# Performance work log

Hardware: AMD Instinct MI355X
Metric: run time of the kernel (lower is better)

The kernel has to match this reference:

```python
import jax, jax.numpy as jnp
import numpy as np

WIN = 7
DIM = 384
HEADS = 12
HEAD_DIM = DIM // HEADS


def relative_position_index(win):
    ch = np.arange(win)
    cw = np.arange(win)
    coords = np.stack(np.meshgrid(ch, cw, indexing='ij'))  # [2,w,w]
    cf = coords.reshape(2, -1)
    rel = cf[:, :, None] - cf[:, None, :]  # [2,ww,ww]
    rel = rel.transpose(1, 2, 0)
    rel[:, :, 0] += win - 1
    rel[:, :, 1] += win - 1
    rel[:, :, 0] *= 2 * win - 1
    return jnp.array(rel.sum(-1), dtype=jnp.int32)  # [ww,ww]


def setup_inputs() -> dict:
    key = jax.random.key(0)
    ks = jax.random.split(key, 9)
    B, S = 1024, WIN * WIN
    M = 16  # windows per image
    s = 1.0 / np.sqrt(DIM)
    return {
        'hidden_states': jax.random.normal(ks[0], (B, S, DIM), jnp.float32),
        'attention_mask': jax.random.normal(ks[1], (M, S, S), jnp.float32),
        'Wq': jax.random.normal(ks[2], (DIM, DIM), jnp.float32) * s,
        'bq': jnp.zeros((DIM,), jnp.float32),
        'Wk': jax.random.normal(ks[3], (DIM, DIM), jnp.float32) * s,
        'bk': jnp.zeros((DIM,), jnp.float32),
        'Wv': jax.random.normal(ks[4], (DIM, DIM), jnp.float32) * s,
        'bv': jnp.zeros((DIM,), jnp.float32),
        'rel_bias_table': jax.random.normal(ks[5], ((2 * WIN - 1) ** 2, HEADS), jnp.float32) * 0.02,
        'rel_index': relative_position_index(WIN),
    }


def reference(hidden_states, attention_mask, Wq, bq, Wk, bk, Wv, bv, rel_bias_table, rel_index):
    B, S, _ = hidden_states.shape
    q = (hidden_states @ Wq + bq).reshape(B, S, HEADS, HEAD_DIM)
    k = (hidden_states @ Wk + bk).reshape(B, S, HEADS, HEAD_DIM)
    v = (hidden_states @ Wv + bv).reshape(B, S, HEADS, HEAD_DIM)
    q = q / jnp.sqrt(jnp.float32(HEAD_DIM)).astype(q.dtype)
    attn = jnp.einsum('bqhd,bkhd->bhqk', q, k)  # [B,H,S,S]
    # relative position bias: gather + reshape + transpose -> [1,H,S,S]
    bias = rel_bias_table[rel_index.reshape(-1)].reshape(S, S, HEADS)
    attn = attn + jnp.transpose(bias, (2, 0, 1))[None]
    # shifted-window mask add: [B//M, M, H, S, S]
    Mw = attention_mask.shape[0]
    attn = attn.reshape(B // Mw, Mw, HEADS, S, S) + attention_mask[None, :, None, :, :]
    attn = attn.reshape(B, HEADS, S, S)
    attn = jax.nn.softmax(attn, axis=-1)
    out = jnp.einsum('bhqk,bkhd->bqhd', attn, v).reshape(B, S, DIM)
    return out
```

## Files before the change

kernel.cpp:

```cpp
#include <hip/hip_runtime.h>

typedef __attribute__((ext_vector_type(8))) short short8;
typedef __attribute__((ext_vector_type(4))) float f32x4;
typedef __attribute__((ext_vector_type(4))) int i32x4;

__device__ __forceinline__ unsigned short f2bf(float f) {
  unsigned u = __builtin_bit_cast(unsigned, f);
  u += 0x7fffu + ((u >> 16) & 1u);
  return (unsigned short)(u >> 16);
}

__global__ __launch_bounds__(256) void k_prepw(const float* __restrict__ Wq, const float* __restrict__ Wk,
                                               const float* __restrict__ Wv, const float* __restrict__ bq,
                                               const float* __restrict__ bk, const float* __restrict__ bv,
                                               unsigned short* __restrict__ Wt, float* __restrict__ bvec) {
  int i = blockIdx.x * 256 + threadIdx.x;
  int n = i / 384, k = i - n * 384;
  int which = n / 384;
  int c = n - which * 384;
  const float* W = (which == 0) ? Wq : (which == 1) ? Wk : Wv;
  Wt[i] = f2bf(W[k * 384 + c]);
  if (k == 0) {
    const float* bb = (which == 0) ? bq : (which == 1) ? bk : bv;
    bvec[n] = bb[c];
  }
}

__global__ __launch_bounds__(256) void k_prept(const float* __restrict__ tab, const int* __restrict__ ridx,
                                               const float* __restrict__ am, float* __restrict__ T) {
  int i = blockIdx.x * 256 + threadIdx.x;
  int lane = i & 63;
  int rest = i >> 6;
  int ik = rest & 3, jq = (rest >> 2) & 3, wh = rest >> 4;
  int h = wh % 12, w = wh / 12;
  int lr = lane & 15, lg = lane >> 4;
  int q = jq * 16 + lr;
  f32x4 v;
  #pragma unroll
  for (int r = 0; r < 4; ++r) {
    int k = ik * 16 + lg * 4 + r;
    v[r] = (q < 49 && k < 49) ? tab[ridx[q * 49 + k] * 12 + h] + am[w * 2401 + q * 49 + k] : 0.f;
  }
  *(f32x4*)(T + (size_t)i * 4) = v;
}

__global__ __launch_bounds__(768, 3) void k_mega(const float* __restrict__ X,
                                                 const unsigned short* __restrict__ Wt,
                                                 const float* __restrict__ bvec,
                                                 const float* __restrict__ T,
                                                 float* __restrict__ out) {
  extern __shared__ unsigned short pool[];
  const int w = blockIdx.x;
  const int tid = threadIdx.x;
  const int lane = tid & 63, wid = tid >> 6;
  const int lr = lane & 15, lg = lane >> 4;
  char* poolB = (char*)pool;

  #pragma unroll
  for (int it = 0; it < 4; ++it) {
    int c = tid + 768 * it;
    int row = c / 48, c8 = c - row * 48;
    short8 v = {0, 0, 0, 0, 0, 0, 0, 0};
    if (row < 49) {
      const float* p = X + ((size_t)(w * 49 + row)) * 384 + c8 * 8;
      f32x4 f0 = *(const f32x4*)p;
      f32x4 f1 = *(const f32x4*)(p + 4);
      v[0] = (short)f2bf(f0[0]); v[1] = (short)f2bf(f0[1]); v[2] = (short)f2bf(f0[2]); v[3] = (short)f2bf(f0[3]);
      v[4] = (short)f2bf(f1[0]); v[5] = (short)f2bf(f1[1]); v[6] = (short)f2bf(f1[2]); v[7] = (short)f2bf(f1[3]);
    }
    *(short8*)(poolB + row * 768 + ((c8 * 16) ^ ((row & 7) << 4))) = v;
  }
  __syncthreads();

  const unsigned swz = (unsigned)((lr & 7) << 4);
  unsigned hq[16], hk[16], hv[16];
  {
    f32x4 acc[3][4][2] = {};
    const unsigned short* Bg0 = Wt + ((size_t)(0 * 384 + wid * 32 + lr)) * 384;
    const unsigned short* Bg1 = Wt + ((size_t)(1 * 384 + wid * 32 + lr)) * 384;
    const unsigned short* Bg2 = Wt + ((size_t)(2 * 384 + wid * 32 + lr)) * 384;
    short8 aC[4], bC[3][2], bN[3][2];
    bC[0][0] = *(const short8*)(Bg0 + lg * 8);
    bC[0][1] = *(const short8*)(Bg0 + 16 * 384 + lg * 8);
    bC[1][0] = *(const short8*)(Bg1 + lg * 8);
    bC[1][1] = *(const short8*)(Bg1 + 16 * 384 + lg * 8);
    bC[2][0] = *(const short8*)(Bg2 + lg * 8);
    bC[2][1] = *(const short8*)(Bg2 + 16 * 384 + lg * 8);
    #pragma unroll 2
    for (int k = 0; k < 12; ++k) {
      if (k < 11) {
        int ko = (k + 1) * 32 + lg * 8;
        bN[0][0] = *(const short8*)(Bg0 + ko);
        bN[0][1] = *(const short8*)(Bg0 + 16 * 384 + ko);
        bN[1][0] = *(const short8*)(Bg1 + ko);
        bN[1][1] = *(const short8*)(Bg1 + 16 * 384 + ko);
        bN[2][0] = *(const short8*)(Bg2 + ko);
        bN[2][1] = *(const short8*)(Bg2 + 16 * 384 + ko);
      }
      #pragma unroll
      for (int mi = 0; mi < 4; ++mi)
        aC[mi] = *(const short8*)(poolB + (16 * mi + lr) * 768 + (unsigned)((k * 64 + lg * 16) ^ swz));
      #pragma unroll
      for (int p = 0; p < 3; ++p)
        #pragma unroll
        for (int mi = 0; mi < 4; ++mi)
          #pragma unroll
          for (int ni = 0; ni < 2; ++ni)
            acc[p][mi][ni] = __builtin_amdgcn_mfma_f32_16x16x32_bf16(aC[mi], bC[p][ni], acc[p][mi][ni], 0, 0, 0);
      #pragma unroll
      for (int p = 0; p < 3; ++p) { bC[p][0] = bN[p][0]; bC[p][1] = bN[p][1]; }
    }
    #pragma unroll
    for (int p = 0; p < 3; ++p) {
      float scl = (p == 0) ? 0.17677669529663687f : 1.0f;
      unsigned* hd = (p == 0) ? hq : (p == 1) ? hk : hv;
      float b0 = bvec[p * 384 + wid * 32 + lr];
      float b1 = bvec[p * 384 + wid * 32 + 16 + lr];
      #pragma unroll
      for (int mi = 0; mi < 4; ++mi)
        #pragma unroll
        for (int ni = 0; ni < 2; ++ni) {
          float bb = ni ? b1 : b0;
          float v0 = (acc[p][mi][ni][0] + bb) * scl;
          float v1 = (acc[p][mi][ni][1] + bb) * scl;
          float v2 = (acc[p][mi][ni][2] + bb) * scl;
          float v3 = (acc[p][mi][ni][3] + bb) * scl;
          hd[(mi * 2 + ni) * 2 + 0] = (unsigned)f2bf(v0) | ((unsigned)f2bf(v1) << 16);
          hd[(mi * 2 + ni) * 2 + 1] = (unsigned)f2bf(v2) | ((unsigned)f2bf(v3) << 16);
        }
    }
  }
  __syncthreads();

  unsigned short* reg = pool + wid * 6400;
  unsigned short* Qs = reg;
  unsigned short* Ks = reg + 1984;
  unsigned short* Vt = reg + 4096;
  char* Pb = (char*)reg;
  #pragma unroll
  for (int mi = 0; mi < 4; ++mi)
    #pragma unroll
    for (int ni = 0; ni < 2; ++ni) {
      int d = ni * 16 + lr;
      #pragma unroll
      for (int e = 0; e < 2; ++e) {
        int s0 = 16 * mi + 4 * lg + 2 * e;
        *(unsigned*)&Vt[d * 72 + s0] = hv[(mi * 2 + ni) * 2 + e];
      }
      #pragma unroll
      for (int r = 0; r < 4; ++r) {
        int s = 16 * mi + 4 * lg + r;
        if (s < 49) {
          unsigned short qv = (unsigned short)(hq[(mi * 2 + ni) * 2 + (r >> 1)] >> ((r & 1) * 16));
          unsigned short kv = (unsigned short)(hk[(mi * 2 + ni) * 2 + (r >> 1)] >> ((r & 1) * 16));
          Qs[s * 40 + d] = qv;
          Ks[s * 40 + d] = kv;
        }
      }
    }

  short8 qf[4], kf[4];
  #pragma unroll
  for (int t = 0; t < 4; ++t) {
    int rq = t * 16 + lr; if (rq > 48) rq = 48;
    qf[t] = *(const short8*)&Qs[rq * 40 + lg * 8];
    kf[t] = *(const short8*)&Ks[rq * 40 + lg * 8];
  }
  f32x4 sc[4][4] = {};
  #pragma unroll
  for (int ik = 0; ik < 4; ++ik)
    #pragma unroll
    for (int jq = 0; jq < 4; ++jq)
      sc[ik][jq] = __builtin_amdgcn_mfma_f32_16x16x32_bf16(kf[ik], qf[jq], sc[ik][jq], 0, 0, 0);

  const float* Tb = T + ((size_t)((w & 15) * 12 + wid)) * 4096;
  #pragma unroll
  for (int jq = 0; jq < 4; ++jq) {
    #pragma unroll
    for (int ik = 0; ik < 4; ++ik) {
      f32x4 tv = *(const f32x4*)(Tb + ((jq * 4 + ik) * 64 + lane) * 4);
      #pragma unroll
      for (int r = 0; r < 4; ++r) {
        float v = sc[ik][jq][r] + tv[r];
        if (ik == 3) {
          if (r == 0) v = (lg == 0) ? v : -1e30f;
          else v = -1e30f;
        }
        sc[ik][jq][r] = v;
      }
    }
    float m = -1e30f;
    #pragma unroll
    for (int ik = 0; ik < 4; ++ik)
      #pragma unroll
      for (int r = 0; r < 4; ++r) m = fmaxf(m, sc[ik][jq][r]);
    m = fmaxf(m, __shfl_xor(m, 16));
    m = fmaxf(m, __shfl_xor(m, 32));
    float s = 0.f;
    #pragma unroll
    for (int ik = 0; ik < 4; ++ik)
      #pragma unroll
      for (int r = 0; r < 4; ++r) {
        float e = __expf(sc[ik][jq][r] - m);
        sc[ik][jq][r] = e;
        s += e;
      }
    s += __shfl_xor(s, 16);
    s += __shfl_xor(s, 32);
    float iv = 1.0f / s;
    int q = jq * 16 + lr;
    #pragma unroll
    for (int ik = 0; ik < 4; ++ik) {
      unsigned d0 = (unsigned)f2bf(sc[ik][jq][0] * iv) | ((unsigned)f2bf(sc[ik][jq][1] * iv) << 16);
      unsigned d1 = (unsigned)f2bf(sc[ik][jq][2] * iv) | ((unsigned)f2bf(sc[ik][jq][3] * iv) << 16);
      unsigned off = (unsigned)(q * 128 + ik * 32 + lg * 8) ^ ((unsigned)(lr & 7) << 4);
      *(uint2*)(Pb + off) = make_uint2(d0, d1);
    }
  }

  short8 vf[2][2];
  #pragma unroll
  for (int kk = 0; kk < 2; ++kk)
    #pragma unroll
    for (int nl = 0; nl < 2; ++nl)
      vf[kk][nl] = *(const short8*)&Vt[(nl * 16 + lr) * 72 + kk * 32 + lg * 8];
  f32x4 ao[4][2] = {};
  #pragma unroll
  for (int i = 0; i < 4; ++i) {
    short8 pf[2];
    #pragma unroll
    for (int kk = 0; kk < 2; ++kk) {
      unsigned off = (unsigned)((i * 16 + lr) * 128 + (kk * 4 + lg) * 16) ^ ((unsigned)(lr & 7) << 4);
      pf[kk] = *(const short8*)(Pb + off);
    }
    #pragma unroll
    for (int nl = 0; nl < 2; ++nl)
      #pragma unroll
      for (int kk = 0; kk < 2; ++kk)
        ao[i][nl] = __builtin_amdgcn_mfma_f32_16x16x32_bf16(pf[kk], vf[kk][nl], ao[i][nl], 0, 0, 0);
  }

  #pragma unroll
  for (int i = 0; i < 4; ++i) {
    #pragma unroll
    for (int j2 = 0; j2 < 4; ++j2) {
      int q = i * 16 + lg * 4 + j2;
      if (q < 49) {
        #pragma unroll
        for (int nl = 0; nl < 2; ++nl) {
          int d = nl * 16 + lr;
          out[((size_t)(w * 49 + q)) * 384 + wid * 32 + d] = ao[i][nl][j2];
        }
      }
    }
  }
}

extern "C" void kernel_launch(void* const* d_in, const int* in_sizes, int n_in,
                              void* d_out, int out_size, void* d_ws, size_t ws_size,
                              hipStream_t stream) {
  const float* hs  = (const float*)d_in[0];
  const float* am  = (const float*)d_in[1];
  const float* Wq  = (const float*)d_in[2];
  const float* bq  = (const float*)d_in[3];
  const float* Wk  = (const float*)d_in[4];
  const float* bk  = (const float*)d_in[5];
  const float* Wv  = (const float*)d_in[6];
  const float* bv  = (const float*)d_in[7];
  const float* tab = (const float*)d_in[8];
  const int*   rix = (const int*)d_in[9];
  float* out = (float*)d_out;
  char* ws = (char*)d_ws;

  size_t o = 0;
  auto alloc = [&](size_t bytes) { size_t r = o; o = (o + bytes + 255) & ~(size_t)255; return r; };
  unsigned short* Wt   = (unsigned short*)(ws + alloc(1152ull * 384 * 2));
  float*          bvec = (float*)(ws + alloc(1152ull * 4));
  float*          Tt   = (float*)(ws + alloc(192ull * 4096 * 4));
  (void)ws_size; (void)in_sizes; (void)n_in; (void)out_size;

  hipFuncSetAttribute((const void*)k_mega, hipFuncAttributeMaxDynamicSharedMemorySize, 153600);

  k_prepw<<<1728, 256, 0, stream>>>(Wq, Wk, Wv, bq, bk, bv, Wt, bvec);
  k_prept<<<768, 256, 0, stream>>>(tab, rix, am, Tt);
  k_mega<<<1024, 768, 153600, stream>>>(hs, Wt, bvec, Tt, out);
}
```

Baseline: 296.4 us.

## Split each window across two blocks of six heads and restructure QKV GEMM loop

Each 12-head window is now handled by two 384-thread blocks, each owning 6 heads, so shared memory per block halves and two blocks can be resident per CU. The QKV projection loop now processes one projection at a time with a 4-deep rotating prefetch buffer for weight fragments, and wraps the MFMA bursts in s_setprio. The intent is to let the staging, GEMM and attention phases of different blocks overlap, and to ease register pressure. In exchange, each window's input rows are loaded from global memory and converted to bf16 twice, once per block.

```diff
diff --git a/kernel.cpp b/kernel.cpp
--- a/kernel.cpp
+++ b/kernel.cpp
@@ -2,7 +2,6 @@
 
 typedef __attribute__((ext_vector_type(8))) short short8;
 typedef __attribute__((ext_vector_type(4))) float f32x4;
-typedef __attribute__((ext_vector_type(4))) int i32x4;
 
 __device__ __forceinline__ unsigned short f2bf(float f) {
   unsigned u = __builtin_bit_cast(unsigned, f);
@@ -44,21 +43,23 @@
   *(f32x4*)(T + (size_t)i * 4) = v;
 }
 
-__global__ __launch_bounds__(768, 3) void k_mega(const float* __restrict__ X,
+__global__ __launch_bounds__(384, 3) void k_mega(const float* __restrict__ X,
                                                  const unsigned short* __restrict__ Wt,
                                                  const float* __restrict__ bvec,
                                                  const float* __restrict__ T,
                                                  float* __restrict__ out) {
   extern __shared__ unsigned short pool[];
-  const int w = blockIdx.x;
+  const int bid = blockIdx.x;
+  const int w = bid >> 1, half = bid & 1;
   const int tid = threadIdx.x;
   const int lane = tid & 63, wid = tid >> 6;
+  const int head = half * 6 + wid;
   const int lr = lane & 15, lg = lane >> 4;
   char* poolB = (char*)pool;
 
   #pragma unroll
-  for (int it = 0; it < 4; ++it) {
-    int c = tid + 768 * it;
+  for (int it = 0; it < 8; ++it) {
+    int c = tid + 384 * it;
     int row = c / 48, c8 = c - row * 48;
     short8 v = {0, 0, 0, 0, 0, 0, 0, 0};
     if (row < 49) {
@@ -74,61 +75,50 @@
 
   const unsigned swz = (unsigned)((lr & 7) << 4);
   unsigned hq[16], hk[16], hv[16];
-  {
-    f32x4 acc[3][4][2] = {};
-    const unsigned short* Bg0 = Wt + ((size_t)(0 * 384 + wid * 32 + lr)) * 384;
-    const unsigned short* Bg1 = Wt + ((size_t)(1 * 384 + wid * 32 + lr)) * 384;
-    const unsigned short* Bg2 = Wt + ((size_t)(2 * 384 + wid * 32 + lr)) * 384;
-    short8 aC[4], bC[3][2], bN[3][2];
-    bC[0][0] = *(const short8*)(Bg0 + lg * 8);
-    bC[0][1] = *(const short8*)(Bg0 + 16 * 384 + lg * 8);
-    bC[1][0] = *(const short8*)(Bg1 + lg * 8);
-    bC[1][1] = *(const short8*)(Bg1 + 16 * 384 + lg * 8);
-    bC[2][0] = *(const short8*)(Bg2 + lg * 8);
-    bC[2][1] = *(const short8*)(Bg2 + 16 * 384 + lg * 8);
-    #pragma unroll 2
+  #pragma unroll
+  for (int p = 0; p < 3; ++p) {
+    const unsigned short* Bg = Wt + ((size_t)(p * 384 + head * 32 + lr)) * 384 + lg * 8;
+    f32x4 acc[4][2] = {};
+    short8 bB[4][2];
+    #pragma unroll
+    for (int k0 = 0; k0 < 3; ++k0) {
+      bB[k0][0] = *(const short8*)(Bg + k0 * 32);
+      bB[k0][1] = *(const short8*)(Bg + 16 * 384 + k0 * 32);
+    }
+    #pragma unroll
     for (int k = 0; k < 12; ++k) {
-      if (k < 11) {
-        int ko = (k + 1) * 32 + lg * 8;
-        bN[0][0] = *(const short8*)(Bg0 + ko);
-        bN[0][1] = *(const short8*)(Bg0 + 16 * 384 + ko);
-        bN[1][0] = *(const short8*)(Bg1 + ko);
-        bN[1][1] = *(const short8*)(Bg1 + 16 * 384 + ko);
-        bN[2][0] = *(const short8*)(Bg2 + ko);
-        bN[2][1] = *(const short8*)(Bg2 + 16 * 384 + ko);
-      }
+      if (k + 3 < 12) {
+        bB[(k + 3) & 3][0] = *(const short8*)(Bg + (k + 3) * 32);
+        bB[(k + 3) & 3][1] = *(const short8*)(Bg + 16 * 384 + (k + 3) * 32);
+      }
+      short8 aC[4];
       #pragma unroll
       for (int mi = 0; mi < 4; ++mi)
         aC[mi] = *(const short8*)(poolB + (16 * mi + lr) * 768 + (unsigned)((k * 64 + lg * 16) ^ swz));
-      #pragma unroll
-      for (int p = 0; p < 3; ++p)
-        #pragma unroll
-        for (int mi = 0; mi < 4; ++mi)
-          #pragma unroll
-          for (int ni = 0; ni < 2; ++ni)
-            acc[p][mi][ni] = __builtin_amdgcn_mfma_f32_16x16x32_bf16(aC[mi], bC[p][ni], acc[p][mi][ni], 0, 0, 0);
-      #pragma unroll
-      for (int p = 0; p < 3; ++p) { bC[p][0] = bN[p][0]; bC[p][1] = bN[p][1]; }
-    }
-    #pragma unroll
-    for (int p = 0; p < 3; ++p) {
-      float scl = (p == 0) ? 0.17677669529663687f : 1.0f;
-      unsigned* hd = (p == 0) ? hq : (p == 1) ? hk : hv;
-      float b0 = bvec[p * 384 + wid * 32 + lr];
-      float b1 = bvec[p * 384 + wid * 32 + 16 + lr];
+      __builtin_amdgcn_s_setprio(1);
       #pragma unroll
       for (int mi = 0; mi < 4; ++mi)
         #pragma unroll
-        for (int ni = 0; ni < 2; ++ni) {
-          float bb = ni ? b1 : b0;
-          float v0 = (acc[p][mi][ni][0] + bb) * scl;
-          float v1 = (acc[p][mi][ni][1] + bb) * scl;
-          float v2 = (acc[p][mi][ni][2] + bb) * scl;
-          float v3 = (acc[p][mi][ni][3] + bb) * scl;
-          hd[(mi * 2 + ni) * 2 + 0] = (unsigned)f2bf(v0) | ((unsigned)f2bf(v1) << 16);
-          hd[(mi * 2 + ni) * 2 + 1] = (unsigned)f2bf(v2) | ((unsigned)f2bf(v3) << 16);
-        }
-    }
+        for (int ni = 0; ni < 2; ++ni)
+          acc[mi][ni] = __builtin_amdgcn_mfma_f32_16x16x32_bf16(aC[mi], bB[k & 3][ni], acc[mi][ni], 0, 0, 0);
+      __builtin_amdgcn_s_setprio(0);
+    }
+    float scl = (p == 0) ? 0.17677669529663687f : 1.0f;
+    unsigned* hd = (p == 0) ? hq : (p == 1) ? hk : hv;
+    float b0 = bvec[p * 384 + head * 32 + lr];
+    float b1 = bvec[p * 384 + head * 32 + 16 + lr];
+    #pragma unroll
+    for (int mi = 0; mi < 4; ++mi)
+      #pragma unroll
+      for (int ni = 0; ni < 2; ++ni) {
+        float bb = ni ? b1 : b0;
+        float v0 = (acc[mi][ni][0] + bb) * scl;
+        float v1 = (acc[mi][ni][1] + bb) * scl;
+        float v2 = (acc[mi][ni][2] + bb) * scl;
+        float v3 = (acc[mi][ni][3] + bb) * scl;
+        hd[(mi * 2 + ni) * 2 + 0] = (unsigned)f2bf(v0) | ((unsigned)f2bf(v1) << 16);
+        hd[(mi * 2 + ni) * 2 + 1] = (unsigned)f2bf(v2) | ((unsigned)f2bf(v3) << 16);
+      }
   }
   __syncthreads();
 
@@ -173,7 +163,7 @@
     for (int jq = 0; jq < 4; ++jq)
       sc[ik][jq] = __builtin_amdgcn_mfma_f32_16x16x32_bf16(kf[ik], qf[jq], sc[ik][jq], 0, 0, 0);
 
-  const float* Tb = T + ((size_t)((w & 15) * 12 + wid)) * 4096;
+  const float* Tb = T + ((size_t)((w & 15) * 12 + head)) * 4096;
   #pragma unroll
   for (int jq = 0; jq < 4; ++jq) {
     #pragma unroll
@@ -249,7 +239,7 @@
         #pragma unroll
         for (int nl = 0; nl < 2; ++nl) {
           int d = nl * 16 + lr;
-          out[((size_t)(w * 49 + q)) * 384 + wid * 32 + d] = ao[i][nl][j2];
+          out[((size_t)(w * 49 + q)) * 384 + head * 32 + d] = ao[i][nl][j2];
         }
       }
     }
@@ -279,9 +269,9 @@
   float*          Tt   = (float*)(ws + alloc(192ull * 4096 * 4));
   (void)ws_size; (void)in_sizes; (void)n_in; (void)out_size;
 
-  hipFuncSetAttribute((const void*)k_mega, hipFuncAttributeMaxDynamicSharedMemorySize, 153600);
+  hipFuncSetAttribute((const void*)k_mega, hipFuncAttributeMaxDynamicSharedMemorySize, 76800);
 
   k_prepw<<<1728, 256, 0, stream>>>(Wq, Wk, Wv, bq, bk, bv, Wt, bvec);
   k_prept<<<768, 256, 0, stream>>>(tab, rix, am, Tt);
-  k_mega<<<1024, 768, 153600, stream>>>(hs, Wt, bvec, Tt, out);
-}
+  k_mega<<<2048, 384, 76800, stream>>>(hs, Wt, bvec, Tt, out);
+}
```

Measured after the change: 318.5 us. 1.07x slower.
